# Kernel tuning notes

Hardware: AMD Instinct MI355X
Metric: run time of the kernel (lower is better)

Reference implementation:

```python
import jax, jax.numpy as jnp
import numpy as np
from jax import lax

B, L_IN, DEC_LEN = 1024, 2048, 64
H = 128            # hidden_size
CARD, EMB = 200, 16  # categorical feature cardinality / embedding dim
VDIM = 4
IN_SIZE = EMB + 1 + 1  # cat-embed + continuous feat (Linear(1,1)) + target value


def setup_inputs() -> dict:
    key = jax.random.key(0)
    k = jax.random.split(key, 19)
    s = 1.0 / np.sqrt(H)  # torch LSTM/Linear default init scale
    u = lambda kk, shape: jax.random.uniform(kk, shape, minval=-s, maxval=s, dtype=jnp.float32)
    return {
        "cat_in": jax.random.randint(k[0], (B, L_IN), 0, CARD, dtype=jnp.int32),
        "cont_in": jax.random.normal(k[1], (B, L_IN, 1), dtype=jnp.float32),
        "X_in": jax.random.normal(k[2], (B, L_IN, 1), dtype=jnp.float32),
        "cat_out": jax.random.randint(k[3], (B, DEC_LEN), 0, CARD, dtype=jnp.int32),
        "cont_out": jax.random.normal(k[4], (B, DEC_LEN, 1), dtype=jnp.float32),
        # learned params
        "emb_table": jax.random.normal(k[5], (CARD, EMB), dtype=jnp.float32) * 0.02,
        "cont_w": jax.random.normal(k[6], (1, 1), dtype=jnp.float32) * 0.5,  # Linear(1,1,bias=False)
        "Wih_e": u(k[7], (4 * H, IN_SIZE)),
        "Whh_e": u(k[8], (4 * H, H)),
        "b_e": u(k[9], (4 * H,)),   # b_ih + b_hh folded together
        "Wih_d": u(k[10], (4 * H, IN_SIZE)),
        "Whh_d": u(k[11], (4 * H, H)),
        "b_d": u(k[12], (4 * H,)),
        "Wm": u(k[13], (1, H)), "bm": u(k[14], (1,)),
        "Ws": u(k[15], (1, H)), "bs": u(k[16], (1,)),
        "Wv": u(k[17], (VDIM, H)), "bv": u(k[18], (VDIM,)),
    }


def _lstm_cell(x, h, c, Wih, Whh, b):
    # torch gate order: i, f, g, o
    gates = x @ Wih.T + h @ Whh.T + b  # [B, 4H]
    i, f, g, o = jnp.split(gates, 4, axis=-1)
    c_new = jax.nn.sigmoid(f) * c + jax.nn.sigmoid(i) * jnp.tanh(g)
    h_new = jax.nn.sigmoid(o) * jnp.tanh(c_new)
    return h_new, c_new


def reference(cat_in, cont_in, X_in, cat_out, cont_out, emb_table, cont_w,
              Wih_e, Whh_e, b_e, Wih_d, Whh_d, b_d, Wm, bm, Ws, bs, Wv, bv):
    w00 = cont_w[0, 0]
    # feature embedding: Embedding for categorical, Linear(1,1,no bias) for continuous
    feats_in_embed = jnp.concatenate([emb_table[cat_in], cont_in * w00], axis=-1)  # [B,L,EMB+1]
    enc_in = jnp.concatenate([feats_in_embed, X_in], axis=-1)                      # [B,L,IN_SIZE]

    h0 = jnp.zeros((X_in.shape[0], H), dtype=X_in.dtype)

    def enc_step(carry, xt):
        h, c = carry
        return _lstm_cell(xt, h, c, Wih_e, Whh_e, b_e), None

    # encoder outputs are unused downstream; only the final (h, c) state matters
    (h, c), _ = lax.scan(enc_step, (h0, h0), jnp.swapaxes(enc_in, 0, 1))

    feats_out_embed = jnp.concatenate([emb_table[cat_out], cont_out * w00], axis=-1)  # [B,D,EMB+1]

    def dec_step(carry, feats_next):
        h, c, x_prev, f_prev = carry
        xt = jnp.concatenate([f_prev, x_prev], axis=-1)  # [B, IN_SIZE]
        h, c = _lstm_cell(xt, h, c, Wih_d, Whh_d, b_d)
        mu = h @ Wm.T + bm                     # [B,1]
        std = jax.nn.softplus(h @ Ws.T + bs)   # [B,1]
        v = h @ Wv.T + bv                      # [B,VDIM]
        return (h, c, mu, feats_next), (mu, std, v)

    init = (h, c, X_in[:, -1, :], feats_in_embed[:, -1, :])
    _, (means, stds, vs) = lax.scan(dec_step, init, jnp.swapaxes(feats_out_embed, 0, 1))
    # [D,B,*] -> [B,D,*]
    return (jnp.swapaxes(means, 0, 1), jnp.swapaxes(stds, 0, 1), jnp.swapaxes(vs, 0, 1))
```

## Files before the change

### kernel.cpp

```cpp
#include <hip/hip_runtime.h>
#include <math.h>

typedef _Float16 half8 __attribute__((ext_vector_type(8)));
typedef float float4v __attribute__((ext_vector_type(4)));

constexpr int Lc   = 2048;
constexpr int DECc = 64;
constexpr int Hc   = 128;
constexpr int EMBc = 16;
constexpr int INc  = 18;
constexpr int NBc  = 4;
constexpr int NTc  = 512;
constexpr int KT   = 5;
constexpr int CARD = 200;
constexpr int ZS   = 160;

__device__ __forceinline__ float rcp_(float x) { return __builtin_amdgcn_rcpf(x); }
__device__ __forceinline__ float sigm(float x) { return rcp_(1.0f + __expf(-x)); }
__device__ __forceinline__ float tanh_(float x) { return 2.0f * rcp_(1.0f + __expf(-2.0f * x)) - 1.0f; }
__device__ __forceinline__ float softplus_(float x) { return __logf(1.0f + __expf(x)); }

__device__ __forceinline__ float sel4(float4v v, int q) {
    const float a = (q & 1) ? v[1] : v[0];
    const float b = (q & 1) ? v[3] : v[2];
    return (q & 2) ? b : a;
}


__global__ __launch_bounds__(NTc, 1) void rnnar_kernel(
    const int*   __restrict__ cat_in,  const float* __restrict__ cont_in,
    const float* __restrict__ X_in,    const int*   __restrict__ cat_out,
    const float* __restrict__ cont_out,const float* __restrict__ emb_table,
    const float* __restrict__ cont_w,
    const float* __restrict__ Wih_e, const float* __restrict__ Whh_e, const float* __restrict__ b_e,
    const float* __restrict__ Wih_d, const float* __restrict__ Whh_d, const float* __restrict__ b_d,
    const float* __restrict__ Wm, const float* __restrict__ bm,
    const float* __restrict__ Ws, const float* __restrict__ bs,
    const float* __restrict__ Wv, const float* __restrict__ bv,
    float* __restrict__ out)
{
    __shared__ _Float16      z_lds[2][NBc * ZS];
    __shared__ _Float16      emb_lds[CARD * EMBc];
    __shared__ _Float16      xs0[NBc * Lc];
    __shared__ _Float16      xs1[NBc * Lc];
    __shared__ _Float16      xo_lds[NBc * DECc];
    __shared__ unsigned char catb[NBc * Lc];
    __shared__ unsigned char catob[NBc * DECc];
    __shared__ float         h32_lds[NBc * 132];
    __shared__ float         wh_lds[6 * Hc];
    __shared__ float         hb_lds[8];

    const int tid  = threadIdx.x;
    const int lane = tid & 63;
    const int wv   = tid >> 6;
    const int q    = lane >> 4;
    const int col  = lane & 15;
    const int cell = 16 * wv + col;
    const int b0   = blockIdx.x * NBc;
    const float w00 = cont_w[0];

    const int xk = tid >> 2, xb = tid & 3;

    {
        int* z32 = (int*)&z_lds[0][0];
        for (int i = tid; i < NBc * ZS; i += NTc) z32[i] = 0;
    }
    for (int i = tid; i < NBc * Lc; i += NTc) {
        const int b = i >> 11, t = i & (Lc - 1);
        catb[i] = (unsigned char)cat_in[(b0 + b) * Lc + t];
        xs0[i]  = (_Float16)(cont_in[(b0 + b) * Lc + t] * w00);
        xs1[i]  = (_Float16)(X_in[(b0 + b) * Lc + t]);
    }
    if (tid < NBc * DECc) {
        const int b = tid >> 6, t = tid & 63;
        catob[tid]  = (unsigned char)cat_out[(b0 + b) * DECc + t];
        xo_lds[tid] = (_Float16)(cont_out[(b0 + b) * DECc + t] * w00);
    }
    for (int i = tid; i < CARD * EMBc; i += NTc) emb_lds[i] = (_Float16)emb_table[i];
    for (int i = tid; i < 6 * Hc; i += NTc) {
        const int o = i >> 7, k = i & 127;
        wh_lds[i] = (o == 0) ? Wm[k] : (o == 1) ? Ws[k] : Wv[(o - 2) * Hc + k];
    }
    if (tid == 0) { hb_lds[0] = bm[0]; hb_lds[1] = bs[0]; }
    if (tid < 4)  { hb_lds[2 + tid] = bv[tid]; }

    half8 Bf[4][KT];
    float bias_s[4];
    #define LOAD_T(WIH, WHH, BB)                                               \
    {                                                                          \
        _Pragma("unroll")                                                      \
        for (int gt = 0; gt < 4; ++gt) {                                       \
            const int row = gt * Hc + cell;                                    \
            _Pragma("unroll")                                                  \
            for (int kt = 0; kt < KT; ++kt) {                                  \
                half8 f;                                                       \
                _Pragma("unroll")                                              \
                for (int j = 0; j < 8; ++j) {                                  \
                    const int k = 32 * kt + 8 * q + j;                         \
                    float v = 0.0f;                                            \
                    if (k < INc)            v = WIH[row * INc + k];            \
                    else if (k < INc + Hc)  v = WHH[row * Hc + (k - INc)];     \
                    f[j] = (_Float16)v;                                        \
                }                                                              \
                Bf[gt][kt] = f;                                                \
            }                                                                  \
            bias_s[gt] = BB[row];                                              \
        }                                                                      \
    }

    LOAD_T(Wih_e, Whh_e, b_e);
    __syncthreads();

    if (tid < INc * NBc) {
        _Float16 v;
        if (xk < EMBc)       v = emb_lds[(int)catb[xb * Lc] * EMBc + xk];
        else if (xk == EMBc) v = xs0[xb * Lc];
        else                 v = xs1[xb * Lc];
        z_lds[0][xb * ZS + xk] = v;
    }
    __syncthreads();

    int p = 0;
    float c_reg = 0.f;

    for (int t = 0; t < Lc; ++t) {
        const _Float16* zr = &z_lds[p][0];
        _Float16*       zw = &z_lds[p ^ 1][0];

        const _Float16* ap = zr + (col & 3) * ZS + 8 * q;
        half8 Az[KT];
        #pragma unroll
        for (int kt = 0; kt < KT; ++kt) Az[kt] = *(const half8*)(ap + 32 * kt);

        float4v acc[4];
        #pragma unroll
        for (int gt = 0; gt < 4; ++gt) {
            float4v a = {bias_s[gt], bias_s[gt], bias_s[gt], bias_s[gt]};
            #pragma unroll
            for (int kt = 0; kt < KT; ++kt)
                a = __builtin_amdgcn_mfma_f32_16x16x32_f16(Az[kt], Bf[gt][kt], a, 0, 0, 0);
            acc[gt] = a;
        }

        const float gi = sel4(acc[0], q);
        const float gf = sel4(acc[1], q);
        const float gg = sel4(acc[2], q);
        const float go = sel4(acc[3], q);

        const float cn = sigm(gf) * c_reg + sigm(gi) * tanh_(gg);
        c_reg = cn;
        zw[q * ZS + INc + cell] = (_Float16)(sigm(go) * tanh_(cn));

        if (tid < INc * NBc) {
            const int t1 = (t + 1 < Lc) ? t + 1 : Lc - 1;
            _Float16 v;
            if (xk < EMBc)       v = emb_lds[(int)catb[xb * Lc + t1] * EMBc + xk];
            else if (xk == EMBc) v = xs0[xb * Lc + t1];
            else                 v = xs1[xb * Lc + t1];
            zw[xb * ZS + xk] = v;
        }
        __syncthreads();
        p ^= 1;
    }

    LOAD_T(Wih_d, Whh_d, b_d);
    const float bm0 = hb_lds[0], bs0 = hb_lds[1];

    for (int t = 0; t < DECc; ++t) {
        const _Float16* zr = &z_lds[p][0];
        _Float16*       zw = &z_lds[p ^ 1][0];

        const _Float16* ap = zr + (col & 3) * ZS + 8 * q;
        half8 Az[KT];
        #pragma unroll
        for (int kt = 0; kt < KT; ++kt) Az[kt] = *(const half8*)(ap + 32 * kt);

        float4v acc[4];
        #pragma unroll
        for (int gt = 0; gt < 4; ++gt) {
            float4v a = {bias_s[gt], bias_s[gt], bias_s[gt], bias_s[gt]};
            #pragma unroll
            for (int kt = 0; kt < KT; ++kt)
                a = __builtin_amdgcn_mfma_f32_16x16x32_f16(Az[kt], Bf[gt][kt], a, 0, 0, 0);
            acc[gt] = a;
        }

        const float gi = sel4(acc[0], q);
        const float gf = sel4(acc[1], q);
        const float gg = sel4(acc[2], q);
        const float go = sel4(acc[3], q);

        const float cn = sigm(gf) * c_reg + sigm(gi) * tanh_(gg);
        c_reg = cn;
        const float hv = sigm(go) * tanh_(cn);
        zw[q * ZS + INc + cell] = (_Float16)hv;
        h32_lds[q * 132 + cell] = hv;

        if (tid < INc * NBc && xk < INc - 1) {
            _Float16 v;
            if (xk < EMBc) v = emb_lds[(int)catob[xb * DECc + t] * EMBc + xk];
            else           v = xo_lds[xb * DECc + t];
            zw[xb * ZS + xk] = v;
        }
        __syncthreads();

        if (tid < 384) {
            const int grp = tid >> 4;
            const int l16 = tid & 15;
            const int b   = grp & 3, o = grp >> 2;
            float s = 0.0f;
            #pragma unroll
            for (int j = 0; j < 8; ++j) {
                const int k = l16 + 16 * j;
                s += wh_lds[o * Hc + k] * h32_lds[b * 132 + k];
            }
            s += __shfl_xor(s, 1);
            s += __shfl_xor(s, 2);
            s += __shfl_xor(s, 4);
            s += __shfl_xor(s, 8);
            if (l16 == 0) {
                const int gb = b0 + b;
                if (o == 0) {
                    const float mu = s + bm0;
                    out[gb * DECc + t] = mu;
                    zw[b * ZS + (INc - 1)] = (_Float16)mu;
                } else if (o == 1) {
                    out[65536 + gb * DECc + t] = softplus_(s + bs0);
                } else {
                    out[131072 + (gb * DECc + t) * 4 + (o - 2)] = s + hb_lds[2 + (o - 2)];
                }
            }
        }
        __syncthreads();
        p ^= 1;
    }
    #undef LOAD_T
}

extern "C" void kernel_launch(void* const* d_in, const int* in_sizes, int n_in,
                              void* d_out, int out_size, void* d_ws, size_t ws_size,
                              hipStream_t stream) {
    rnnar_kernel<<<1024 / NBc, NTc, 0, stream>>>(
        (const int*)d_in[0],   (const float*)d_in[1],  (const float*)d_in[2],
        (const int*)d_in[3],   (const float*)d_in[4],  (const float*)d_in[5],
        (const float*)d_in[6],
        (const float*)d_in[7], (const float*)d_in[8],  (const float*)d_in[9],
        (const float*)d_in[10],(const float*)d_in[11], (const float*)d_in[12],
        (const float*)d_in[13],(const float*)d_in[14],
        (const float*)d_in[15],(const float*)d_in[16],
        (const float*)d_in[17],(const float*)d_in[18],
        (float*)d_out);
}
```

Measured before the change: 1.150 ms.

## Precompute input-projection MFMA for next step off the recurrent critical path

Reorders the K dimension so the hidden state occupies the first 128 columns and the input features the last tile. The input projection for step t+1 is computed with one MFMA per gate right after step t's recurrent MFMAs and used as the accumulator seed. This shortens the dependent chain per step from 5 to 4 MFMAs and removes the per-step scalar LDS staging of input features. In the decoder the fed-back mean is applied as a scalar FMA using a cached weight column, and it is now kept in fp32 rather than fp16. The cost is extra registers for the precomputed accumulators.

```diff
diff --git a/kernel.cpp b/kernel.cpp
--- a/kernel.cpp
+++ b/kernel.cpp
@@ -11,9 +11,9 @@
 constexpr int INc  = 18;
 constexpr int NBc  = 4;
 constexpr int NTc  = 512;
-constexpr int KT   = 5;
 constexpr int CARD = 200;
 constexpr int ZS   = 160;
+
 
 __device__ __forceinline__ float rcp_(float x) { return __builtin_amdgcn_rcpf(x); }
 __device__ __forceinline__ float sigm(float x) { return rcp_(1.0f + __expf(-x)); }
@@ -49,6 +49,7 @@
     __shared__ float         h32_lds[NBc * 132];
     __shared__ float         wh_lds[6 * Hc];
     __shared__ float         hb_lds[8];
+    __shared__ float         mu_lds[4];
 
     const int tid  = threadIdx.x;
     const int lane = tid & 63;
@@ -56,10 +57,9 @@
     const int q    = lane >> 4;
     const int col  = lane & 15;
     const int cell = 16 * wv + col;
+    const int bx   = col & 3;
     const int b0   = blockIdx.x * NBc;
     const float w00 = cont_w[0];
-
-    const int xk = tid >> 2, xb = tid & 3;
 
     {
         int* z32 = (int*)&z_lds[0][0];
@@ -82,43 +82,54 @@
         wh_lds[i] = (o == 0) ? Wm[k] : (o == 1) ? Ws[k] : Wv[(o - 2) * Hc + k];
     }
     if (tid == 0) { hb_lds[0] = bm[0]; hb_lds[1] = bs[0]; }
-    if (tid < 4)  { hb_lds[2 + tid] = bv[tid]; }
-
-    half8 Bf[4][KT];
+    if (tid < 4)  { hb_lds[2 + tid] = bv[tid]; mu_lds[tid] = 0.0f; }
+
+    half8 Bf[4][5];
     float bias_s[4];
+    float w17_s[4];
     #define LOAD_T(WIH, WHH, BB)                                               \
     {                                                                          \
         _Pragma("unroll")                                                      \
         for (int gt = 0; gt < 4; ++gt) {                                       \
             const int row = gt * Hc + cell;                                    \
             _Pragma("unroll")                                                  \
-            for (int kt = 0; kt < KT; ++kt) {                                  \
+            for (int kt = 0; kt < 5; ++kt) {                                   \
                 half8 f;                                                       \
                 _Pragma("unroll")                                              \
                 for (int j = 0; j < 8; ++j) {                                  \
                     const int k = 32 * kt + 8 * q + j;                         \
                     float v = 0.0f;                                            \
-                    if (k < INc)            v = WIH[row * INc + k];            \
-                    else if (k < INc + Hc)  v = WHH[row * Hc + (k - INc)];     \
+                    if (k < Hc)             v = WHH[row * Hc + k];             \
+                    else if (k < Hc + INc)  v = WIH[row * INc + (k - Hc)];     \
                     f[j] = (_Float16)v;                                        \
                 }                                                              \
                 Bf[gt][kt] = f;                                                \
             }                                                                  \
             bias_s[gt] = BB[row];                                              \
+            w17_s[gt]  = WIH[row * INc + 17];                                  \
         }                                                                      \
     }
 
     LOAD_T(Wih_e, Whh_e, b_e);
     __syncthreads();
 
-    if (tid < INc * NBc) {
-        _Float16 v;
-        if (xk < EMBc)       v = emb_lds[(int)catb[xb * Lc] * EMBc + xk];
-        else if (xk == EMBc) v = xs0[xb * Lc];
-        else                 v = xs1[xb * Lc];
-        z_lds[0][xb * ZS + xk] = v;
-    }
-    __syncthreads();
+    float4v acc_pre[4];
+
+    #define PRE_ENC(T1)                                                        \
+    {                                                                          \
+        const int t1 = (T1);                                                   \
+        half8 ax;                                                              \
+        _Pragma("unroll") for (int j = 0; j < 8; ++j) ax[j] = (_Float16)0.0f;  \
+        if (q < 2)       ax = *(const half8*)&emb_lds[(int)catb[bx * Lc + t1] * EMBc + 8 * q]; \
+        else if (q == 2) { ax[0] = xs0[bx * Lc + t1]; ax[1] = xs1[bx * Lc + t1]; } \
+        _Pragma("unroll")                                                      \
+        for (int gt = 0; gt < 4; ++gt) {                                       \
+            float4v a = {bias_s[gt], bias_s[gt], bias_s[gt], bias_s[gt]};      \
+            acc_pre[gt] = __builtin_amdgcn_mfma_f32_16x16x32_f16(ax, Bf[gt][4], a, 0, 0, 0); \
+        }                                                                      \
+    }
+
+    PRE_ENC(0);
 
     int p = 0;
     float c_reg = 0.f;
@@ -127,20 +138,22 @@
         const _Float16* zr = &z_lds[p][0];
         _Float16*       zw = &z_lds[p ^ 1][0];
 
-        const _Float16* ap = zr + (col & 3) * ZS + 8 * q;
-        half8 Az[KT];
-        #pragma unroll
-        for (int kt = 0; kt < KT; ++kt) Az[kt] = *(const half8*)(ap + 32 * kt);
+        const _Float16* ap = zr + bx * ZS + 8 * q;
+        half8 Az[4];
+        #pragma unroll
+        for (int kt = 0; kt < 4; ++kt) Az[kt] = *(const half8*)(ap + 32 * kt);
 
         float4v acc[4];
         #pragma unroll
         for (int gt = 0; gt < 4; ++gt) {
-            float4v a = {bias_s[gt], bias_s[gt], bias_s[gt], bias_s[gt]};
-            #pragma unroll
-            for (int kt = 0; kt < KT; ++kt)
+            float4v a = acc_pre[gt];
+            #pragma unroll
+            for (int kt = 0; kt < 4; ++kt)
                 a = __builtin_amdgcn_mfma_f32_16x16x32_f16(Az[kt], Bf[gt][kt], a, 0, 0, 0);
             acc[gt] = a;
         }
+
+        PRE_ENC((t + 1 < Lc) ? t + 1 : Lc - 1);
 
         const float gi = sel4(acc[0], q);
         const float gf = sel4(acc[1], q);
@@ -149,59 +162,75 @@
 
         const float cn = sigm(gf) * c_reg + sigm(gi) * tanh_(gg);
         c_reg = cn;
-        zw[q * ZS + INc + cell] = (_Float16)(sigm(go) * tanh_(cn));
-
-        if (tid < INc * NBc) {
-            const int t1 = (t + 1 < Lc) ? t + 1 : Lc - 1;
-            _Float16 v;
-            if (xk < EMBc)       v = emb_lds[(int)catb[xb * Lc + t1] * EMBc + xk];
-            else if (xk == EMBc) v = xs0[xb * Lc + t1];
-            else                 v = xs1[xb * Lc + t1];
-            zw[xb * ZS + xk] = v;
-        }
+        zw[q * ZS + cell] = (_Float16)(sigm(go) * tanh_(cn));
+
         __syncthreads();
         p ^= 1;
     }
 
     LOAD_T(Wih_d, Whh_d, b_d);
     const float bm0 = hb_lds[0], bs0 = hb_lds[1];
+
+    {
+        const int t1 = Lc - 1;
+        half8 ax;
+        #pragma unroll
+        for (int j = 0; j < 8; ++j) ax[j] = (_Float16)0.0f;
+        if (q < 2)       ax = *(const half8*)&emb_lds[(int)catb[bx * Lc + t1] * EMBc + 8 * q];
+        else if (q == 2) { ax[0] = xs0[bx * Lc + t1]; ax[1] = xs1[bx * Lc + t1]; }
+        #pragma unroll
+        for (int gt = 0; gt < 4; ++gt) {
+            float4v a = {bias_s[gt], bias_s[gt], bias_s[gt], bias_s[gt]};
+            acc_pre[gt] = __builtin_amdgcn_mfma_f32_16x16x32_f16(ax, Bf[gt][4], a, 0, 0, 0);
+        }
+    }
+    __syncthreads();
 
     for (int t = 0; t < DECc; ++t) {
         const _Float16* zr = &z_lds[p][0];
         _Float16*       zw = &z_lds[p ^ 1][0];
 
-        const _Float16* ap = zr + (col & 3) * ZS + 8 * q;
-        half8 Az[KT];
-        #pragma unroll
-        for (int kt = 0; kt < KT; ++kt) Az[kt] = *(const half8*)(ap + 32 * kt);
+        const float muq = mu_lds[q];
+
+        const _Float16* ap = zr + bx * ZS + 8 * q;
+        half8 Az[4];
+        #pragma unroll
+        for (int kt = 0; kt < 4; ++kt) Az[kt] = *(const half8*)(ap + 32 * kt);
 
         float4v acc[4];
         #pragma unroll
         for (int gt = 0; gt < 4; ++gt) {
-            float4v a = {bias_s[gt], bias_s[gt], bias_s[gt], bias_s[gt]};
-            #pragma unroll
-            for (int kt = 0; kt < KT; ++kt)
+            float4v a = acc_pre[gt];
+            #pragma unroll
+            for (int kt = 0; kt < 4; ++kt)
                 a = __builtin_amdgcn_mfma_f32_16x16x32_f16(Az[kt], Bf[gt][kt], a, 0, 0, 0);
             acc[gt] = a;
         }
 
-        const float gi = sel4(acc[0], q);
-        const float gf = sel4(acc[1], q);
-        const float gg = sel4(acc[2], q);
-        const float go = sel4(acc[3], q);
+        {
+            half8 ax;
+            #pragma unroll
+            for (int j = 0; j < 8; ++j) ax[j] = (_Float16)0.0f;
+            if (q < 2)       ax = *(const half8*)&emb_lds[(int)catob[bx * DECc + t] * EMBc + 8 * q];
+            else if (q == 2) ax[0] = xo_lds[bx * DECc + t];
+            #pragma unroll
+            for (int gt = 0; gt < 4; ++gt) {
+                float4v a = {bias_s[gt], bias_s[gt], bias_s[gt], bias_s[gt]};
+                acc_pre[gt] = __builtin_amdgcn_mfma_f32_16x16x32_f16(ax, Bf[gt][4], a, 0, 0, 0);
+            }
+        }
+
+        const float gi = sel4(acc[0], q) + muq * w17_s[0];
+        const float gf = sel4(acc[1], q) + muq * w17_s[1];
+        const float gg = sel4(acc[2], q) + muq * w17_s[2];
+        const float go = sel4(acc[3], q) + muq * w17_s[3];
 
         const float cn = sigm(gf) * c_reg + sigm(gi) * tanh_(gg);
         c_reg = cn;
         const float hv = sigm(go) * tanh_(cn);
-        zw[q * ZS + INc + cell] = (_Float16)hv;
+        zw[q * ZS + cell] = (_Float16)hv;
         h32_lds[q * 132 + cell] = hv;
 
-        if (tid < INc * NBc && xk < INc - 1) {
-            _Float16 v;
-            if (xk < EMBc) v = emb_lds[(int)catob[xb * DECc + t] * EMBc + xk];
-            else           v = xo_lds[xb * DECc + t];
-            zw[xb * ZS + xk] = v;
-        }
         __syncthreads();
 
         if (tid < 384) {
@@ -223,7 +252,7 @@
                 if (o == 0) {
                     const float mu = s + bm0;
                     out[gb * DECc + t] = mu;
-                    zw[b * ZS + (INc - 1)] = (_Float16)mu;
+                    mu_lds[b] = mu;
                 } else if (o == 1) {
                     out[65536 + gb * DECc + t] = softplus_(s + bs0);
                 } else {
@@ -235,6 +264,7 @@
         p ^= 1;
     }
     #undef LOAD_T
+    #undef PRE_ENC
 }
 
 extern "C" void kernel_launch(void* const* d_in, const int* in_sizes, int n_in,
```

Result: slower. 1.380 ms (+20.0%).
